# Optimization experiments

Measured on AMD Instinct MI355X. Metric: run time of the kernel, lower is better.

Reference implementation:

```python
import jax, jax.numpy as jnp
import numpy as np

NUM_NET = 5
N = 10000        # nodes per net
E = 160000       # edges per net
B = 512          # molecule graphs per batch
FXD = 62         # node feature dim
FXT = 954        # cell feature dim
D = 128          # output_dim
H1 = 10          # heads in first GATConv


def setup_inputs() -> dict:
    key = jax.random.key(0)
    ks = iter(jax.random.split(key, 64))
    f32 = jnp.float32
    p = lambda shape, scale=0.05: jax.random.normal(next(ks), shape, dtype=f32) * scale
    inp = {}
    inp['x1'] = jax.random.normal(next(ks), (NUM_NET, N, FXD), dtype=f32)
    inp['ei1'] = jax.random.randint(next(ks), (NUM_NET, 2, E), 0, N, dtype=jnp.int32)
    b = ((jnp.arange(N) * B) // N).astype(jnp.int32)  # sorted, no empty graphs
    inp['batch1'] = jnp.broadcast_to(b, (NUM_NET, N))
    inp['x2'] = jax.random.normal(next(ks), (NUM_NET, N, FXD), dtype=f32)
    inp['ei2'] = jax.random.randint(next(ks), (NUM_NET, 2, E), 0, N, dtype=jnp.int32)
    inp['batch2'] = jnp.broadcast_to(b, (NUM_NET, N))
    inp['cell'] = jax.random.normal(next(ks), (B, FXT), dtype=f32)
    # per-net GAT params (stacked over NUM_NET)
    inp['W1'] = p((NUM_NET, H1 * D, FXD))
    inp['a1s'] = p((NUM_NET, H1, D)); inp['a1d'] = p((NUM_NET, H1, D))
    inp['b1'] = p((NUM_NET, H1 * D))
    inp['W2'] = p((NUM_NET, D, H1 * D))
    inp['a2s'] = p((NUM_NET, 1, D)); inp['a2d'] = p((NUM_NET, 1, D))
    inp['b2'] = p((NUM_NET, D))
    inp['Wg'] = p((NUM_NET, D, D)); inp['bg'] = p((NUM_NET, D))
    # cell reduction MLP 954->2048->512->256
    inp['Wr1'] = p((2048, FXT)); inp['br1'] = p((2048,))
    inp['Wr2'] = p((512, 2048)); inp['br2'] = p((512,))
    inp['Wr3'] = p((2 * D, 512)); inp['br3'] = p((2 * D,))
    # head MLP 512->2048->512->128->2
    inp['Wf1'] = p((2048, 4 * D)); inp['bf1'] = p((2048,))
    inp['Wf2'] = p((512, 2048)); inp['bf2'] = p((512,))
    inp['Wf3'] = p((128, 512)); inp['bf3'] = p((128,))
    inp['Wo'] = p((2, 128)); inp['bo'] = p((2,))
    return inp


def _gat(x, src, dst, W, a_s, a_d, b):
    # PyG GATConv (eval): linear -> per-head attention logits -> segment softmax over dst -> scatter-sum
    n = x.shape[0]
    H, C = a_s.shape
    h = (x @ W.T).reshape(n, H, C)
    al = (h * a_s).sum(-1)   # [n, H] source term
    ar = (h * a_d).sum(-1)   # [n, H] dest term
    e = jax.nn.leaky_relu(al[src] + ar[dst], negative_slope=0.2)  # [Ee, H]
    m = jax.ops.segment_max(e, dst, num_segments=n)               # self-loops -> no empty segments
    pe = jnp.exp(e - m[dst])
    s = jax.ops.segment_sum(pe, dst, num_segments=n)
    alpha = pe / s[dst]
    out = jax.ops.segment_sum(h[src] * alpha[:, :, None], dst, num_segments=n)
    return out.reshape(n, H * C) + b


def _branch(x, ei, batch, W1, a1s, a1d, b1, W2, a2s, a2d, b2, Wg, bg):
    n = x.shape[0]
    loops = jnp.arange(n, dtype=ei.dtype)  # add_self_loops=True in PyG GATConv
    src = jnp.concatenate([ei[0], loops])
    dst = jnp.concatenate([ei[1], loops])
    h = jax.nn.elu(_gat(x, src, dst, W1, a1s, a1d, b1))
    h = jax.nn.elu(_gat(h, src, dst, W2, a2s, a2d, b2))
    g = jax.ops.segment_max(h, batch, num_segments=B)  # global max pool
    return jax.nn.relu(g @ Wg.T + bg)


def _l2n(v):
    return v / jnp.clip(jnp.linalg.norm(v, axis=1, keepdims=True), 1e-12)


def reference(x1, ei1, batch1, x2, ei2, batch2, cell,
              W1, a1s, a1d, b1, W2, a2s, a2d, b2, Wg, bg,
              Wr1, br1, Wr2, br2, Wr3, br3,
              Wf1, bf1, Wf2, bf2, Wf3, bf3, Wo, bo):
    x11 = jnp.zeros((B, D), dtype=x1.dtype)
    x22 = jnp.zeros((B, D), dtype=x2.dtype)
    for i in range(NUM_NET):
        pr = (W1[i], a1s[i], a1d[i], b1[i], W2[i], a2s[i], a2d[i], b2[i], Wg[i], bg[i])
        x11 = x11 + _branch(x1[i], ei1[i], batch1[i], *pr) / NUM_NET
        x22 = x22 + _branch(x2[i], ei2[i], batch2[i], *pr) / NUM_NET
    c = _l2n(cell)
    c = jax.nn.relu(c @ Wr1.T + br1)
    c = jax.nn.relu(c @ Wr2.T + br2)
    c = jax.nn.relu(c @ Wr3.T + br3)
    xc = _l2n(jnp.concatenate([x11, x22, c], axis=1))
    xc = jax.nn.relu(xc @ Wf1.T + bf1)
    xc = jax.nn.relu(xc @ Wf2.T + bf2)
    xc = jax.nn.relu(xc @ Wf3.T + bf3)
    return xc @ Wo.T + bo
```

## Files before the change

### kernel.cpp

```cpp
#include <hip/hip_runtime.h>
#include <hip/hip_bf16.h>
#include <math.h>

#define NUM_NET 5
#define NN 10000
#define NE 160000
#define BB 512
#define FXD 62
#define FXT 954
#define MP 10112

typedef __bf16 bf16x8 __attribute__((ext_vector_type(8)));
typedef float f32x4 __attribute__((ext_vector_type(4)));
typedef __hip_bfloat16 bf16;

__device__ __forceinline__ float ldf(const void* p, size_t i) {
  return ((const float*)p)[i];
}
__device__ __forceinline__ float lky(float v) { return v > 0.f ? v : 0.2f * v; }
__device__ __forceinline__ float eluf(float v) { return v > 0.f ? v : (__expf(v) - 1.f); }
__device__ __forceinline__ unsigned int packbf(float a, float b) {
  __hip_bfloat162 t;
  t.x = __float2bfloat16(a);
  t.y = __float2bfloat16(b);
  return *(unsigned int*)&t;
}

struct ConvDesc {
  const void* src;
  bf16* dst;
  int M, K, Mp, Kp, mult, add, batch, pad;
};
struct ConvTable { ConvDesc d[11]; };

__global__ void convert_all_kernel(ConvTable tab) {
  ConvDesc c = tab.d[blockIdx.z];
  int b = blockIdx.y;
  if (b >= c.batch) return;
  int wave = threadIdx.x >> 6, lane = threadIdx.x & 63;
  int r = blockIdx.x * 4 + wave;
  if (r >= c.Mp) return;
  const float* srow = (const float*)c.src + ((size_t)b * c.M + r) * c.K;
  bf16* drow = c.dst + (((size_t)(b * c.mult + c.add)) * c.Mp + r) * c.Kp;
  bool rowok = r < c.M;
  for (int k = lane; k < c.Kp; k += 64) {
    float v = (rowok && k < c.K) ? srow[k] : 0.f;
    drow[k] = __float2bfloat16(v);
  }
}

__global__ void hist_kernel(const int* __restrict__ ei1, const int* __restrict__ ei2,
                            int* __restrict__ counts) {
  int z = blockIdx.z;
  int br = z & 1, net = z >> 1;
  const int* base = (br ? ei2 : ei1) + (size_t)net * 2 * NE;
  const int* dst = base + NE;
  int* cnt = counts + (size_t)z * NN;
  int i = blockIdx.x * 256 + threadIdx.x;
  if (i < NE) atomicAdd(&cnt[dst[i]], 1);
}

__global__ void scan_kernel(const int* __restrict__ counts, int* __restrict__ offs) {
  int z = blockIdx.x;
  counts += (size_t)z * NN;
  offs += (size_t)z * (NN + 1);
  __shared__ int sdata[256];
  __shared__ int s_carry;
  int t = threadIdx.x;
  if (t == 0) { s_carry = 0; offs[0] = 0; }
  __syncthreads();
  for (int base = 0; base < NN; base += 1024) {
    int loc = base + t * 4;
    int v[4];
#pragma unroll
    for (int j = 0; j < 4; j++) v[j] = (loc + j < NN) ? counts[loc + j] : 0;
    int sum4 = v[0] + v[1] + v[2] + v[3];
    sdata[t] = sum4;
    __syncthreads();
    for (int o = 1; o < 256; o <<= 1) {
      int x = (t >= o) ? sdata[t - o] : 0;
      __syncthreads();
      sdata[t] += x;
      __syncthreads();
    }
    int running = sdata[t] - sum4 + s_carry;
#pragma unroll
    for (int j = 0; j < 4; j++) {
      running += v[j];
      if (loc + j < NN) offs[loc + j + 1] = running;
    }
    int tot = sdata[255];
    __syncthreads();
    if (t == 0) s_carry += tot;
    __syncthreads();
  }
}

__global__ void scatter_kernel(const int* __restrict__ ei1, const int* __restrict__ ei2,
                               const int* __restrict__ offs, int* __restrict__ fill,
                               int* __restrict__ csrc) {
  int z = blockIdx.z;
  int br = z & 1, net = z >> 1;
  const int* base = (br ? ei2 : ei1) + (size_t)net * 2 * NE;
  const int* src = base;
  const int* dst = base + NE;
  const int* offz = offs + (size_t)z * (NN + 1);
  int* fillz = fill + (size_t)z * NN;
  int* out = csrc + (size_t)z * NE;
  int i = blockIdx.x * 256 + threadIdx.x;
  if (i < NE) {
    int d = dst[i];
    int p = offz[d] + atomicAdd(&fillz[d], 1);
    out[p] = src[i];
  }
}

__global__ __launch_bounds__(256) void walr_kernel(const void* __restrict__ W1,
                                                   const void* __restrict__ a1s,
                                                   const void* __restrict__ a1d,
                                                   bf16* __restrict__ walrb) {
  int net = blockIdx.x / 10, head = blockIdx.x % 10;
  int t = threadIdx.x, w = t >> 6, k = t & 63;
  __shared__ float ps[8][64];
  float accs = 0.f, accd = 0.f;
  for (int c = w; c < 128; c += 4) {
    float wv = (k < FXD)
        ? ldf(W1, (size_t)net * 1280 * FXD + (size_t)(head * 128 + c) * FXD + k) : 0.f;
    float vs = ldf(a1s, (size_t)net * 1280 + head * 128 + c);
    float vd = ldf(a1d, (size_t)net * 1280 + head * 128 + c);
    accs = fmaf(wv, vs, accs);
    accd = fmaf(wv, vd, accd);
  }
  ps[w][k] = accs;
  ps[4 + w][k] = accd;
  __syncthreads();
  if (w == 0) {
    float s = ps[0][k] + ps[1][k] + ps[2][k] + ps[3][k];
    float dd = ps[4][k] + ps[5][k] + ps[6][k] + ps[7][k];
    walrb[(size_t)net * 4096 + head * 64 + k] = __float2bfloat16(s);
    walrb[(size_t)net * 4096 + (16 + head) * 64 + k] = __float2bfloat16(dd);
  }
}

__global__ __launch_bounds__(256) void alpha_kernel(
    const float* __restrict__ alrA, const int* __restrict__ offsA,
    const int* __restrict__ srcsA, unsigned int* __restrict__ alphaG, int planeBase) {
  int z = blockIdx.z;
  int plane = planeBase + z;
  const float* alr = alrA + (size_t)plane * MP * 32;
  const int* offs = offsA + (size_t)plane * (NN + 1);
  const int* srcs = srcsA + (size_t)plane * NE;
  unsigned int* ag = alphaG + (size_t)z * (NE + NN) * 6;
  int wave = threadIdx.x >> 6, lane = threadIdx.x & 63;
  int d = blockIdx.x * 4 + wave;
  if (d >= NN) return;
  int e0 = offs[d], ne = offs[d + 1] - e0;
  int total = ne + 1;
  float arh[10];
#pragma unroll
  for (int h = 0; h < 10; h++) arh[h] = alr[(size_t)d * 32 + 16 + h];
  if (total <= 64) {
    int sc = (lane < ne) ? srcs[e0 + lane] : d;
    bool act = lane < total;
    const float* ap = &alr[(size_t)sc * 32];
    float v[10], m[10];
#pragma unroll
    for (int h = 0; h < 10; h++) {
      v[h] = act ? lky(ap[h] + arh[h]) : -1e30f;
      m[h] = v[h];
    }
#pragma unroll
    for (int o = 32; o > 0; o >>= 1)
#pragma unroll
      for (int h = 0; h < 10; h++) m[h] = fmaxf(m[h], __shfl_xor(m[h], o));
    float p[10], s[10];
#pragma unroll
    for (int h = 0; h < 10; h++) {
      p[h] = act ? __expf(v[h] - m[h]) : 0.f;
      s[h] = p[h];
    }
#pragma unroll
    for (int o = 32; o > 0; o >>= 1)
#pragma unroll
      for (int h = 0; h < 10; h++) s[h] += __shfl_xor(s[h], o);
    if (act) {
      float inv[10];
#pragma unroll
      for (int h = 0; h < 10; h++) inv[h] = 1.f / s[h];
      unsigned int wv[6];
#pragma unroll
      for (int hp = 0; hp < 5; hp++)
        wv[hp] = packbf(p[2 * hp] * inv[2 * hp], p[2 * hp + 1] * inv[2 * hp + 1]);
      wv[5] = (unsigned int)(d & 15);
      size_t row = (lane < ne) ? (size_t)(e0 + lane) : (size_t)(NE + d);
      unsigned int* rp = ag + row * 6;
#pragma unroll
      for (int j = 0; j < 6; j++) rp[j] = wv[j];
    }
  } else {
    float m[10], s[10];
#pragma unroll
    for (int h = 0; h < 10; h++) { m[h] = -1e30f; s[h] = 0.f; }
    for (int idx = lane; idx < total; idx += 64) {
      int sc = (idx < ne) ? srcs[e0 + idx] : d;
      const float* ap = &alr[(size_t)sc * 32];
#pragma unroll
      for (int h = 0; h < 10; h++) {
        float v = lky(ap[h] + arh[h]);
        if (v > m[h]) { s[h] = s[h] * __expf(m[h] - v) + 1.f; m[h] = v; }
        else s[h] += __expf(v - m[h]);
      }
    }
#pragma unroll
    for (int o = 32; o > 0; o >>= 1)
#pragma unroll
      for (int h = 0; h < 10; h++) {
        float mo = __shfl_xor(m[h], o), so = __shfl_xor(s[h], o);
        if (so > 0.f) {
          if (mo > m[h]) { s[h] = s[h] * __expf(m[h] - mo) + so; m[h] = mo; }
          else s[h] += so * __expf(mo - m[h]);
        }
      }
    for (int idx = lane; idx < total; idx += 64) {
      int sc = (idx < ne) ? srcs[e0 + idx] : d;
      const float* ap = &alr[(size_t)sc * 32];
      unsigned int wv[6];
#pragma unroll
      for (int hp = 0; hp < 5; hp++) {
        float v0 = lky(ap[2 * hp] + arh[2 * hp]);
        float v1 = lky(ap[2 * hp + 1] + arh[2 * hp + 1]);
        wv[hp] = packbf(__expf(v0 - m[2 * hp]) / s[2 * hp],
                        __expf(v1 - m[2 * hp + 1]) / s[2 * hp + 1]);
      }
      wv[5] = (unsigned int)(d & 15);
      size_t row = (idx < ne) ? (size_t)(e0 + idx) : (size_t)(NE + d);
      unsigned int* rp = ag + row * 6;
#pragma unroll
      for (int j = 0; j < 6; j++) rp[j] = wv[j];
    }
  }
}

struct Pref {
  uint4 xv;
  unsigned int a0, a1, a2, a3, a4;
  int dl;
  int av;
};

__device__ __forceinline__ void issue_pref(
    Pref& P, int kb, int e, int fblk, int tid, int nreal, int K_len, int e_begin,
    int d0, const int* __restrict__ srcs, const bf16* __restrict__ xp,
    const unsigned int* __restrict__ ag) {
  int ke = kb + e;
  int src;
  if (ke < nreal) {
    src = srcs[e_begin + ke];
  } else {
    int sl = ke - nreal;
    src = d0 + (sl < 16 ? sl : 0);
  }
  P.xv = *(const uint4*)&xp[(size_t)src * 64 + fblk * 8];
  P.av = 0;
  if (tid < 32 && ke < K_len) {
    P.av = 1;
    size_t row = (ke < nreal) ? (size_t)(e_begin + ke) : (size_t)(NE + d0 + (ke - nreal));
    const unsigned int* rp = ag + row * 6;
    P.a0 = rp[0]; P.a1 = rp[1]; P.a2 = rp[2]; P.a3 = rp[3]; P.a4 = rp[4];
    P.dl = (int)rp[5];
  }
}

__global__ __launch_bounds__(256) void xagg_kernel(
    const bf16* __restrict__ xpadA, const unsigned int* __restrict__ alphaG,
    const int* __restrict__ offsA, const int* __restrict__ srcsA,
    bf16* __restrict__ xagg2, int planeBase) {
  int z = blockIdx.z;
  int plane = planeBase + z;
  bf16* xagg = xagg2 + (size_t)z * 10 * MP * 64;
  int d0 = blockIdx.x * 16;
  int tid = threadIdx.x;

  if (d0 >= NN) {
    uint4 zz; zz.x = zz.y = zz.z = zz.w = 0u;
#pragma unroll
    for (int k = 0; k < 5; k++) {
      int i = tid + k * 256;
      int h = i >> 7, rem = i & 127, row = rem >> 3, seg = rem & 7;
      *(uint4*)&xagg[((size_t)h * MP + d0 + row) * 64 + seg * 8] = zz;
    }
    return;
  }

  const bf16* xp = xpadA + (size_t)plane * MP * 64;
  const int* offs = offsA + (size_t)plane * (NN + 1);
  const int* srcs = srcsA + (size_t)plane * NE;
  const unsigned int* ag = alphaG + (size_t)z * (NE + NN) * 6;

  __shared__ __align__(16) short A_s[10 * 16 * 40];
  __shared__ __align__(16) short Xt_s[64 * 40];

  int e_begin = offs[d0];
  int nreal = offs[d0 + 16] - e_begin;
  int K_len = nreal + 16;

  int e = tid & 31, fblk = tid >> 5;
  int lane = tid & 63, wave = tid >> 6;
  int l15 = lane & 15, quad = lane >> 4;
  int hbase = (wave >> 1) * 5;
  int wcol = (wave & 1) * 32;

  Pref Pn;
  issue_pref(Pn, 0, e, fblk, tid, nreal, K_len, e_begin, d0, srcs, xp, ag);

  {
    f32x4 z4 = (f32x4){0.f, 0.f, 0.f, 0.f};
    for (int i = tid; i < 800; i += 256) ((f32x4*)A_s)[i] = z4;
  }
  f32x4 acc[5][2];
#pragma unroll
  for (int i = 0; i < 5; i++)
#pragma unroll
    for (int j = 0; j < 2; j++) acc[i][j] = (f32x4){0.f, 0.f, 0.f, 0.f};
  int prev_dl = -1;
  __syncthreads();

  for (int kb = 0; kb < K_len; kb += 32) {
    Pref Pc = Pn;
    if (tid < 32) {
      if (prev_dl >= 0) {
#pragma unroll
        for (int h = 0; h < 10; h++) A_s[(h * 16 + prev_dl) * 40 + e] = 0;
      }
      prev_dl = -1;
      if (Pc.av) {
        int dlc = Pc.dl;
        A_s[(0 * 16 + dlc) * 40 + e] = (short)(Pc.a0 & 0xffff);
        A_s[(1 * 16 + dlc) * 40 + e] = (short)(Pc.a0 >> 16);
        A_s[(2 * 16 + dlc) * 40 + e] = (short)(Pc.a1 & 0xffff);
        A_s[(3 * 16 + dlc) * 40 + e] = (short)(Pc.a1 >> 16);
        A_s[(4 * 16 + dlc) * 40 + e] = (short)(Pc.a2 & 0xffff);
        A_s[(5 * 16 + dlc) * 40 + e] = (short)(Pc.a2 >> 16);
        A_s[(6 * 16 + dlc) * 40 + e] = (short)(Pc.a3 & 0xffff);
        A_s[(7 * 16 + dlc) * 40 + e] = (short)(Pc.a3 >> 16);
        A_s[(8 * 16 + dlc) * 40 + e] = (short)(Pc.a4 & 0xffff);
        A_s[(9 * 16 + dlc) * 40 + e] = (short)(Pc.a4 >> 16);
        prev_dl = dlc;
      }
    }
    {
      int fb8 = fblk * 8;
#pragma unroll
      for (int j = 0; j < 4; j++) {
        unsigned int w = ((const unsigned int*)&Pc.xv)[j];
        Xt_s[(fb8 + 2 * j) * 40 + e] = (short)(w & 0xffff);
        Xt_s[(fb8 + 2 * j + 1) * 40 + e] = (short)(w >> 16);
      }
    }
    if (kb + 32 < K_len)
      issue_pref(Pn, kb + 32, e, fblk, tid, nreal, K_len, e_begin, d0, srcs, xp, ag);
    __syncthreads();
    bf16x8 b0 = *(const bf16x8*)&Xt_s[(wcol + l15) * 40 + quad * 8];
    bf16x8 b1 = *(const bf16x8*)&Xt_s[(wcol + 16 + l15) * 40 + quad * 8];
#pragma unroll
    for (int hh = 0; hh < 5; hh++) {
      bf16x8 af = *(const bf16x8*)&A_s[((hbase + hh) * 16 + l15) * 40 + quad * 8];
      acc[hh][0] = __builtin_amdgcn_mfma_f32_16x16x32_bf16(af, b0, acc[hh][0], 0, 0, 0);
      acc[hh][1] = __builtin_amdgcn_mfma_f32_16x16x32_bf16(af, b1, acc[hh][1], 0, 0, 0);
    }
    __syncthreads();
  }

#pragma unroll
  for (int hh = 0; hh < 5; hh++) {
    int h = hbase + hh;
#pragma unroll
    for (int ft = 0; ft < 2; ft++) {
#pragma unroll
      for (int r = 0; r < 4; r++) {
        int drow = d0 + quad * 4 + r;
        xagg[((size_t)h * MP + drow) * 64 + wcol + ft * 16 + l15] =
            __float2bfloat16(acc[hh][ft][r]);
      }
    }
  }
}

__global__ __launch_bounds__(256) void fused_l1l2_kernel(
    const bf16* __restrict__ xagg2, const bf16* __restrict__ W1b,
    const void* __restrict__ b1raw, const bf16* __restrict__ W2b,
    const void* __restrict__ a2s, const void* __restrict__ a2d,
    float* __restrict__ al2A, float* __restrict__ ar2A,
    bf16* __restrict__ h2all, int planeBase) {
  int zz = blockIdx.z;
  int plane = planeBase + zz;
  int net = plane >> 1;
  long ow1 = (long)net * 1280 * 64;
  long ob1 = (long)net * 1280;
  long ow2 = (long)net * 128 * 1280;
  long oa2 = (long)net * 128;
  const bf16* xagg = xagg2 + (size_t)zz * 10 * MP * 64;
  float* al2p = al2A + (size_t)plane * NN;
  float* ar2p = ar2A + (size_t)plane * NN;
  bf16* h2 = h2all + (size_t)plane * MP * 128;
  int r0 = blockIdx.y * 64;
  __shared__ __align__(16) char uraw[52224];
  bf16* Ah = (bf16*)uraw;
  bf16* W1s = Ah + 64 * 72;
  bf16* Ps = (bf16*)uraw;
  bf16* W2s = Ps + 64 * 136;
  __shared__ float s_dot[2][2][32][2];
  int tid = threadIdx.x, lane = tid & 63, wave = tid >> 6;
  int l15 = lane & 15, quad = lane >> 4;
  int rowHalf = wave >> 1, colHalf = wave & 1;
  int wr = rowHalf * 32, wc = colHalf * 64;
  f32x4 acc2[2][4];
#pragma unroll
  for (int i = 0; i < 2; i++)
#pragma unroll
    for (int j = 0; j < 4; j++) acc2[i][j] = (f32x4){0.f, 0.f, 0.f, 0.f};

  for (int h = 0; h < 10; h++) {
    __syncthreads();
    for (int i = tid; i < 512; i += 256) {
      int r = i >> 3, seg = i & 7;
      *(uint4*)&Ah[r * 72 + seg * 8] =
          *(const uint4*)&xagg[((size_t)h * MP + r0 + r) * 64 + seg * 8];
    }
    for (int i = tid; i < 1024; i += 256) {
      int r = i >> 3, seg = i & 7;
      *(uint4*)&W1s[r * 72 + seg * 8] =
          *(const uint4*)&W1b[ow1 + (size_t)(h * 128 + r) * 64 + seg * 8];
    }
    __syncthreads();
    f32x4 acc1[4][2];
#pragma unroll
    for (int i = 0; i < 4; i++)
#pragma unroll
      for (int j = 0; j < 2; j++) acc1[i][j] = (f32x4){0.f, 0.f, 0.f, 0.f};
#pragma unroll
    for (int kc = 0; kc < 2; kc++) {
      bf16x8 af[4], bfr[2];
#pragma unroll
      for (int mi = 0; mi < 4; mi++)
        af[mi] = *(const bf16x8*)&Ah[(mi * 16 + l15) * 72 + kc * 32 + quad * 8];
#pragma unroll
      for (int ni = 0; ni < 2; ni++)
        bfr[ni] = *(const bf16x8*)&W1s[(wave * 32 + ni * 16 + l15) * 72 + kc * 32 + quad * 8];
#pragma unroll
      for (int mi = 0; mi < 4; mi++)
#pragma unroll
        for (int ni = 0; ni < 2; ni++)
          acc1[mi][ni] = __builtin_amdgcn_mfma_f32_16x16x32_bf16(af[mi], bfr[ni], acc1[mi][ni], 0, 0, 0);
    }
    __syncthreads();
#pragma unroll
    for (int ni = 0; ni < 2; ni++) {
      int pcol = wave * 32 + ni * 16 + l15;
      float bv = ldf(b1raw, ob1 + h * 128 + pcol);
#pragma unroll
      for (int mi = 0; mi < 4; mi++)
#pragma unroll
        for (int r = 0; r < 4; r++)
          Ps[(mi * 16 + quad * 4 + r) * 136 + pcol] =
              __float2bfloat16(eluf(acc1[mi][ni][r] + bv));
    }
    for (int i = tid; i < 2048; i += 256) {
      int r = i >> 4, seg = i & 15;
      *(uint4*)&W2s[r * 136 + seg * 8] =
          *(const uint4*)&W2b[ow2 + (size_t)r * 1280 + h * 128 + seg * 8];
    }
    __syncthreads();
#pragma unroll
    for (int kc = 0; kc < 4; kc++) {
      bf16x8 pa[2], pb[4];
#pragma unroll
      for (int mi = 0; mi < 2; mi++)
        pa[mi] = *(const bf16x8*)&Ps[(wr + mi * 16 + l15) * 136 + kc * 32 + quad * 8];
#pragma unroll
      for (int ni = 0; ni < 4; ni++)
        pb[ni] = *(const bf16x8*)&W2s[(wc + ni * 16 + l15) * 136 + kc * 32 + quad * 8];
#pragma unroll
      for (int mi = 0; mi < 2; mi++)
#pragma unroll
        for (int ni = 0; ni < 4; ni++)
          acc2[mi][ni] = __builtin_amdgcn_mfma_f32_16x16x32_bf16(pa[mi], pb[ni], acc2[mi][ni], 0, 0, 0);
    }
  }
  float asv[4], adv[4];
#pragma unroll
  for (int ni = 0; ni < 4; ni++) {
    int col = wc + ni * 16 + l15;
    asv[ni] = ldf(a2s, oa2 + col);
    adv[ni] = ldf(a2d, oa2 + col);
  }
#pragma unroll
  for (int mi = 0; mi < 2; mi++) {
#pragma unroll
    for (int r = 0; r < 4; r++) {
      int rl = mi * 16 + quad * 4 + r;
      int row = r0 + wr + rl;
      float psum = 0.f, pdum = 0.f;
#pragma unroll
      for (int ni = 0; ni < 4; ni++) {
        float v = acc2[mi][ni][r];
        h2[(size_t)row * 128 + wc + ni * 16 + l15] = __float2bfloat16(v);
        psum = fmaf(v, asv[ni], psum);
        pdum = fmaf(v, adv[ni], pdum);
      }
#pragma unroll
      for (int o = 1; o < 16; o <<= 1) {
        psum += __shfl_xor(psum, o);
        pdum += __shfl_xor(pdum, o);
      }
      if (l15 == 0) {
        s_dot[rowHalf][colHalf][rl][0] = psum;
        s_dot[rowHalf][colHalf][rl][1] = pdum;
      }
    }
  }
  __syncthreads();
  if (tid < 64) {
    int row = r0 + tid;
    if (row < NN) {
      int rh = tid >> 5, rl = tid & 31;
      al2p[row] = s_dot[rh][0][rl][0] + s_dot[rh][1][rl][0];
      ar2p[row] = s_dot[rh][0][rl][1] + s_dot[rh][1][rl][1];
    }
  }
}

__global__ __launch_bounds__(256) void mfma_gemm64(
    const bf16* __restrict__ A, long Az, const bf16* __restrict__ B, long Bz, int bdiv,
    const void* __restrict__ bias, long biasoff, long biaszs,
    float* __restrict__ Cf, long Cfz, int ldcf, int accum, int ncols, int brcol,
    bf16* __restrict__ Cb, long Cbz, int ldcb,
    int K, int act, float scale) {
  int z = blockIdx.z;
  int zb = bdiv ? (z >> 1) : z;
  A += (size_t)z * Az;
  B += (size_t)zb * Bz;
  if (Cf) Cf += (size_t)z * Cfz + (size_t)(z & 1) * brcol;
  if (Cb) Cb += (size_t)z * Cbz;
  const bf16* Ag = A + (size_t)blockIdx.y * 64 * K;
  const bf16* Bg = B + (size_t)blockIdx.x * 64 * K;
  __shared__ __align__(16) bf16 Asm[64 * 40];
  __shared__ __align__(16) bf16 Bsm[64 * 40];
  int tid = threadIdx.x;
  int lane = tid & 63, wave = tid >> 6;
  int wr = (wave >> 1) * 32, wc = (wave & 1) * 32;
  int l15 = lane & 15, quad = lane >> 4;
  f32x4 acc[2][2];
#pragma unroll
  for (int i = 0; i < 2; i++)
#pragma unroll
    for (int j = 0; j < 2; j++) acc[i][j] = (f32x4){0.f, 0.f, 0.f, 0.f};
  int isB = tid >> 7;
  int srow = (tid & 127) >> 1, shalf = tid & 1;
  const bf16* G = isB ? Bg : Ag;
  bf16* S = isB ? Bsm : Asm;
  for (int k0 = 0; k0 < K; k0 += 32) {
    const uint4* g = (const uint4*)(G + (size_t)srow * K + k0 + shalf * 16);
    uint4 v0 = g[0], v1 = g[1];
    __syncthreads();
    *(uint4*)&S[srow * 40 + shalf * 16] = v0;
    *(uint4*)&S[srow * 40 + shalf * 16 + 8] = v1;
    __syncthreads();
    bf16x8 af[2], bfr[2];
#pragma unroll
    for (int mi = 0; mi < 2; mi++)
      af[mi] = *(const bf16x8*)&Asm[(wr + mi * 16 + l15) * 40 + quad * 8];
#pragma unroll
    for (int ni = 0; ni < 2; ni++)
      bfr[ni] = *(const bf16x8*)&Bsm[(wc + ni * 16 + l15) * 40 + quad * 8];
#pragma unroll
    for (int mi = 0; mi < 2; mi++)
#pragma unroll
      for (int ni = 0; ni < 2; ni++)
        acc[mi][ni] = __builtin_amdgcn_mfma_f32_16x16x32_bf16(af[mi], bfr[ni], acc[mi][ni], 0, 0, 0);
  }
#pragma unroll
  for (int ni = 0; ni < 2; ni++) {
    int col = blockIdx.x * 64 + wc + ni * 16 + l15;
    if (col >= ncols) continue;
    float bv = bias ? ldf(bias, biasoff + (size_t)zb * biaszs + col) : 0.f;
#pragma unroll
    for (int mi = 0; mi < 2; mi++) {
      int rbase = blockIdx.y * 64 + wr + mi * 16 + quad * 4;
      f32x4 c = acc[mi][ni];
#pragma unroll
      for (int r = 0; r < 4; r++) {
        float v = c[r] + bv;
        if (act == 1) v = fmaxf(v, 0.f);
        else if (act == 2) v = eluf(v);
        v *= scale;
        if (Cf) {
          size_t ci = (size_t)(rbase + r) * ldcf + col;
          if (accum == 1) Cf[ci] += v;
          else if (accum == 2) atomicAdd(&Cf[ci], v);
          else Cf[ci] = v;
        }
        if (Cb) Cb[(size_t)(rbase + r) * ldcb + col] = __float2bfloat16(v);
      }
    }
  }
}

__global__ __launch_bounds__(256) void gat_agg1_kernel(
    const bf16* __restrict__ h2all, const float* __restrict__ alA, const float* __restrict__ arA,
    const int* __restrict__ offsA, const int* __restrict__ srcsA,
    const void* __restrict__ b2, bf16* __restrict__ out2all) {
  int z = blockIdx.z;
  int net = z >> 1;
  const bf16* h = h2all + (size_t)z * MP * 128;
  const float* al = alA + (size_t)z * NN;
  const float* ar = arA + (size_t)z * NN;
  const int* offs = offsA + (size_t)z * (NN + 1);
  const int* srcs = srcsA + (size_t)z * NE;
  __shared__ float2 s_pair[4][64];
  int wave = threadIdx.x >> 6, lane = threadIdx.x & 63;
  int d = blockIdx.x * 4 + wave;
  if (d >= NN) return;
  int e0 = offs[d], ne = offs[d + 1] - e0;
  int total = ne + 1;
  float ard = ar[d];
  float m, s, vcache = -1e30f;
  if (total <= 64) {
    int sc = (lane < ne) ? srcs[e0 + lane] : d;
    bool act = lane < total;
    vcache = act ? lky(al[sc] + ard) : -1e30f;
    m = vcache;
    s = act ? 1.f : 0.f;
#pragma unroll
    for (int o = 32; o > 0; o >>= 1) {
      float mo = __shfl_xor(m, o), so = __shfl_xor(s, o);
      if (so > 0.f) {
        if (mo > m) { s = s * __expf(m - mo) + so; m = mo; }
        else s += so * __expf(mo - m);
      }
    }
  } else {
    m = -1e30f; s = 0.f;
    for (int idx = lane; idx < total; idx += 64) {
      int sc = (idx < ne) ? srcs[e0 + idx] : d;
      float v = lky(al[sc] + ard);
      if (v > m) { s = s * __expf(m - v) + 1.f; m = v; }
      else s += __expf(v - m);
    }
#pragma unroll
    for (int o = 32; o > 0; o >>= 1) {
      float mo = __shfl_xor(m, o), so = __shfl_xor(s, o);
      if (so > 0.f) {
        if (mo > m) { s = s * __expf(m - mo) + so; m = mo; }
        else s += so * __expf(mo - m);
      }
    }
  }
  float inv_s = 1.f / s;
  float acc0 = 0.f, acc1v = 0.f;
  for (int c0 = 0; c0 < total; c0 += 64) {
    int idx = c0 + lane;
    int cnt = min(64, total - c0);
    if (idx < total) {
      int sc = (idx < ne) ? srcs[e0 + idx] : d;
      float v = (total <= 64) ? vcache : lky(al[sc] + ard);
      float a = __expf(v - m) * inv_s;
      s_pair[wave][lane] = make_float2(__int_as_float(sc), a);
    }
    int i = 0;
    for (; i + 2 <= cnt; i += 2) {
      float2 pA = s_pair[wave][i];
      float2 pB = s_pair[wave][i + 1];
      __hip_bfloat162 vA =
          ((const __hip_bfloat162*)(h + (size_t)__float_as_int(pA.x) * 128))[lane];
      __hip_bfloat162 vB =
          ((const __hip_bfloat162*)(h + (size_t)__float_as_int(pB.x) * 128))[lane];
      acc0 = fmaf(__bfloat162float(vA.x), pA.y, acc0);
      acc1v = fmaf(__bfloat162float(vA.y), pA.y, acc1v);
      acc0 = fmaf(__bfloat162float(vB.x), pB.y, acc0);
      acc1v = fmaf(__bfloat162float(vB.y), pB.y, acc1v);
    }
    if (i < cnt) {
      float2 pA = s_pair[wave][i];
      __hip_bfloat162 vA =
          ((const __hip_bfloat162*)(h + (size_t)__float_as_int(pA.x) * 128))[lane];
      acc0 = fmaf(__bfloat162float(vA.x), pA.y, acc0);
      acc1v = fmaf(__bfloat162float(vA.y), pA.y, acc1v);
    }
  }
  float b0 = ldf(b2, (size_t)net * 128 + 2 * lane);
  float b1v = ldf(b2, (size_t)net * 128 + 2 * lane + 1);
  __hip_bfloat162 o;
  o.x = __float2bfloat16(eluf(acc0 + b0));
  o.y = __float2bfloat16(eluf(acc1v + b1v));
  ((__hip_bfloat162*)(out2all + ((size_t)z * NN + d) * 128))[lane] = o;
}

__global__ __launch_bounds__(256) void pool_max_kernel(const bf16* __restrict__ out2all,
                                                       bf16* __restrict__ gall) {
  int z = blockIdx.z;
  const bf16* h = out2all + (size_t)z * NN * 128;
  bf16* g = gall + (size_t)z * BB * 128;
  int wave = threadIdx.x >> 6, lane = threadIdx.x & 63;
  int b = blockIdx.x * 4 + wave;
  if (b >= BB) return;
  int n0 = (b * NN + BB - 1) / BB;
  int n1 = ((b + 1) * NN + BB - 1) / BB;
  if (n1 > NN) n1 = NN;
  float mx = -1e30f, my = -1e30f;
  for (int n = n0; n < n1; n++) {
    __hip_bfloat162 v = ((const __hip_bfloat162*)(h + (size_t)n * 128))[lane];
    mx = fmaxf(mx, __bfloat162float(v.x));
    my = fmaxf(my, __bfloat162float(v.y));
  }
  __hip_bfloat162 o;
  o.x = __float2bfloat16(mx);
  o.y = __float2bfloat16(my);
  ((__hip_bfloat162*)(g + (size_t)b * 128))[lane] = o;
}

__global__ __launch_bounds__(256) void l2norm_b_kernel(const float* __restrict__ x,
                                                       bf16* __restrict__ y, int Din, int Kp) {
  int r = blockIdx.x, t = threadIdx.x;
  __shared__ float red[256];
  float s = 0.f;
  for (int i = t; i < Din; i += 256) {
    float v = x[(size_t)r * Din + i];
    s += v * v;
  }
  red[t] = s;
  __syncthreads();
  for (int o = 128; o > 0; o >>= 1) { if (t < o) red[t] += red[t + o]; __syncthreads(); }
  float inv = 1.f / fmaxf(sqrtf(red[0]), 1e-12f);
  for (int i = t; i < Kp; i += 256) {
    float v = (i < Din) ? x[(size_t)r * Din + i] : 0.f;
    y[(size_t)r * Kp + i] = __float2bfloat16(v * inv);
  }
}

__global__ void final_out_kernel(const float* __restrict__ f3, const void* __restrict__ Wo,
                                 const void* __restrict__ bo, float* __restrict__ out) {
  int r = blockIdx.x;
  int lane = threadIdx.x;
  float x0 = f3[(size_t)r * 128 + lane], x1v = f3[(size_t)r * 128 + 64 + lane];
  float s0 = x0 * ldf(Wo, lane) + x1v * ldf(Wo, 64 + lane);
  float s1 = x0 * ldf(Wo, 128 + lane) + x1v * ldf(Wo, 192 + lane);
#pragma unroll
  for (int o = 32; o > 0; o >>= 1) { s0 += __shfl_down(s0, o); s1 += __shfl_down(s1, o); }
  if (lane == 0) {
    out[r * 2] = s0 + ldf(bo, 0);
    out[r * 2 + 1] = s1 + ldf(bo, 1);
  }
}


extern "C" void kernel_launch(void* const* d_in, const int* in_sizes, int n_in,
                              void* d_out, int out_size, void* d_ws, size_t ws_size,
                              hipStream_t stream) {
  const void* x1 = d_in[0];
  const int* ei1 = (const int*)d_in[1];
  const void* x2 = d_in[3];
  const int* ei2 = (const int*)d_in[4];
  const void* cell = d_in[6];
  const void* W1 = d_in[7];
  const void* a1s = d_in[8];
  const void* a1d = d_in[9];
  const void* b1 = d_in[10];
  const void* W2 = d_in[11];
  const void* a2s = d_in[12];
  const void* a2d = d_in[13];
  const void* b2 = d_in[14];
  const void* Wg = d_in[15];
  const void* bg = d_in[16];
  const void* Wr1 = d_in[17]; const void* br1 = d_in[18];
  const void* Wr2 = d_in[19]; const void* br2 = d_in[20];
  const void* Wr3 = d_in[21]; const void* br3 = d_in[22];
  const void* Wf1 = d_in[23]; const void* bf1 = d_in[24];
  const void* Wf2 = d_in[25]; const void* bf2 = d_in[26];
  const void* Wf3 = d_in[27]; const void* bf3 = d_in[28];
  const void* Wo = d_in[29]; const void* bo = d_in[30];

  char* base = (char*)d_ws;
  size_t off = 0;
  auto alloc = [&](size_t bytes) -> void* {
    void* p = base + off;
    off = (off + bytes + 255) & ~(size_t)255;
    return p;
  };
  bf16* d_xpad = (bf16*)alloc((size_t)10 * MP * 64 * 2);
  bf16* d_W1b = (bf16*)alloc((size_t)5 * 1280 * 64 * 2);
  bf16* d_W2b = (bf16*)alloc((size_t)5 * 128 * 1280 * 2);
  bf16* d_Wgb = (bf16*)alloc((size_t)5 * 128 * 128 * 2);
  bf16* d_Wr1b = (bf16*)alloc((size_t)2048 * 960 * 2);
  bf16* d_Wr2b = (bf16*)alloc((size_t)512 * 2048 * 2);
  bf16* d_Wr3b = (bf16*)alloc((size_t)256 * 512 * 2);
  bf16* d_Wf1b = (bf16*)alloc((size_t)2048 * 512 * 2);
  bf16* d_Wf2b = (bf16*)alloc((size_t)512 * 2048 * 2);
  bf16* d_Wf3b = (bf16*)alloc((size_t)128 * 512 * 2);
  int* d_offs = (int*)alloc((size_t)10 * (NN + 1) * 4);
  int* d_srcs = (int*)alloc((size_t)10 * NE * 4);
  int* d_cnt = (int*)alloc((size_t)10 * NN * 4);
  bf16* d_walrb = (bf16*)alloc((size_t)5 * 64 * 64 * 2);
  float* d_alr = (float*)alloc((size_t)10 * MP * 32 * 4);
  float* d_al2 = (float*)alloc((size_t)20 * NN * 4);
  float* d_ar2 = d_al2 + (size_t)10 * NN;
  bf16* d_h2all = (bf16*)alloc((size_t)10 * MP * 128 * 2);
  unsigned int* d_alphaG = (unsigned int*)alloc((size_t)5 * (NE + NN) * 24);
  char* uni = base + off;
  bf16* d_xagg2 = (bf16*)uni;
  bf16* d_out2all = (bf16*)uni;
  bf16* d_gall = (bf16*)(uni + 25600000);
  float* d_xc = (float*)(uni + 26910720);
  bf16* d_xcb = (bf16*)(uni + 27959296);
  bf16* d_cnb = (bf16*)(uni + 28483584);
  bf16* d_m1b = (bf16*)(uni + 29466624);
  bf16* d_m2b = (bf16*)(uni + 31563776);
  float* d_f3 = (float*)(uni + 32088064);

  ConvTable tab;
  tab.d[0] = {x1, d_xpad, NN, FXD, MP, 64, 2, 0, 5, 0};
  tab.d[1] = {x2, d_xpad, NN, FXD, MP, 64, 2, 1, 5, 0};
  tab.d[2] = {W1, d_W1b, 1280, FXD, 1280, 64, 1, 0, 5, 0};
  tab.d[3] = {W2, d_W2b, 128, 1280, 128, 1280, 1, 0, 5, 0};
  tab.d[4] = {Wg, d_Wgb, 128, 128, 128, 128, 1, 0, 5, 0};
  tab.d[5] = {Wr1, d_Wr1b, 2048, FXT, 2048, 960, 1, 0, 1, 0};
  tab.d[6] = {Wr2, d_Wr2b, 512, 2048, 512, 2048, 1, 0, 1, 0};
  tab.d[7] = {Wr3, d_Wr3b, 256, 512, 256, 512, 1, 0, 1, 0};
  tab.d[8] = {Wf1, d_Wf1b, 2048, 512, 2048, 512, 1, 0, 1, 0};
  tab.d[9] = {Wf2, d_Wf2b, 512, 2048, 512, 2048, 1, 0, 1, 0};
  tab.d[10] = {Wf3, d_Wf3b, 128, 512, 128, 512, 1, 0, 1, 0};
  convert_all_kernel<<<dim3((MP + 3) / 4, 5, 11), 256, 0, stream>>>(tab);

  hipMemsetAsync(d_cnt, 0, (size_t)10 * NN * 4, stream);
  hist_kernel<<<dim3((NE + 255) / 256, 1, 10), 256, 0, stream>>>(ei1, ei2, d_cnt);
  scan_kernel<<<10, 256, 0, stream>>>(d_cnt, d_offs);
  hipMemsetAsync(d_cnt, 0, (size_t)10 * NN * 4, stream);
  scatter_kernel<<<dim3((NE + 255) / 256, 1, 10), 256, 0, stream>>>(ei1, ei2, d_offs, d_cnt, d_srcs);

  walr_kernel<<<50, 256, 0, stream>>>(W1, a1s, a1d, d_walrb);
  mfma_gemm64<<<dim3(1, MP / 64, 10), 256, 0, stream>>>(
      d_xpad, (long)MP * 64, d_walrb, 4096, 1, nullptr, 0, 0,
      d_alr, (long)MP * 32, 32, 0, 32, 0, nullptr, 0, 0, 64, 0, 1.f);

  const int G = 5;
  for (int pb = 0; pb < 10; pb += G) {
    alpha_kernel<<<dim3(NN / 4, 1, G), 256, 0, stream>>>(d_alr, d_offs, d_srcs, d_alphaG, pb);
    xagg_kernel<<<dim3(MP / 16, 1, G), 256, 0, stream>>>(d_xpad, d_alphaG, d_offs, d_srcs, d_xagg2, pb);
    fused_l1l2_kernel<<<dim3(1, MP / 64, G), 256, 0, stream>>>(
        d_xagg2, d_W1b, b1, d_W2b, a2s, a2d, d_al2, d_ar2, d_h2all, pb);
  }

  hipMemsetAsync(d_xc, 0, (size_t)BB * 512 * 4, stream);
  gat_agg1_kernel<<<dim3(2500, 1, 10), 256, 0, stream>>>(
      d_h2all, d_al2, d_ar2, d_offs, d_srcs, b2, d_out2all);
  pool_max_kernel<<<dim3(BB / 4, 1, 10), 256, 0, stream>>>(d_out2all, d_gall);
  mfma_gemm64<<<dim3(2, BB / 64, 10), 256, 0, stream>>>(
      d_gall, (long)BB * 128, d_Wgb, 128 * 128, 1,
      bg, 0, 128,
      d_xc, 0, 512, 2, 128, 128, nullptr, 0, 0, 128, 1, 0.2f);

  l2norm_b_kernel<<<BB, 256, 0, stream>>>((const float*)cell, d_cnb, FXT, 960);
  mfma_gemm64<<<dim3(32, 8, 1), 256, 0, stream>>>(
      d_cnb, 0, d_Wr1b, 0, 0, br1, 0, 0, nullptr, 0, 0, 0, 1 << 30, 0, d_m1b, 0, 2048, 960, 1, 1.f);
  mfma_gemm64<<<dim3(8, 8, 1), 256, 0, stream>>>(
      d_m1b, 0, d_Wr2b, 0, 0, br2, 0, 0, nullptr, 0, 0, 0, 1 << 30, 0, d_m2b, 0, 512, 2048, 1, 1.f);
  mfma_gemm64<<<dim3(4, 8, 1), 256, 0, stream>>>(
      d_m2b, 0, d_Wr3b, 0, 0, br3, 0, 0, d_xc + 256, 0, 512, 0, 1 << 30, 0, nullptr, 0, 0, 512, 1, 1.f);

  l2norm_b_kernel<<<BB, 256, 0, stream>>>(d_xc, d_xcb, 512, 512);
  mfma_gemm64<<<dim3(32, 8, 1), 256, 0, stream>>>(
      d_xcb, 0, d_Wf1b, 0, 0, bf1, 0, 0, nullptr, 0, 0, 0, 1 << 30, 0, d_m1b, 0, 2048, 512, 1, 1.f);
  mfma_gemm64<<<dim3(8, 8, 1), 256, 0, stream>>>(
      d_m1b, 0, d_Wf2b, 0, 0, bf2, 0, 0, nullptr, 0, 0, 0, 1 << 30, 0, d_m2b, 0, 512, 2048, 1, 1.f);
  mfma_gemm64<<<dim3(2, 8, 1), 256, 0, stream>>>(
      d_m2b, 0, d_Wf3b, 0, 0, bf3, 0, 0, d_f3, 0, 128, 0, 1 << 30, 0, nullptr, 0, 0, 512, 1, 1.f);
  final_out_kernel<<<BB, 64, 0, stream>>>(d_f3, Wo, bo, (float*)d_out);
}
```

Before: 1.014 ms.

## Prefetch fused GAT tiles through registers and batch all planes when workspace allows

Inside the fused layer1/layer2 kernel, the next head's xagg and W1 tiles and the current head's W2 tile are now loaded into registers ahead of their LDS stores. This hides global-load latency behind the MFMA work. Separately, the host enlarges the alpha buffer and, if workspace space permits, runs all 10 planes in one group instead of two groups of 5. That cuts launch count and raises per-launch parallelism, at the cost of more register pressure and a larger memory footprint.

Measured after the change: 1.283 ms. 1.27x slower.

```diff
diff --git a/kernel.cpp b/kernel.cpp
--- a/kernel.cpp
+++ b/kernel.cpp
@@ -420,17 +420,34 @@
 #pragma unroll
     for (int j = 0; j < 4; j++) acc2[i][j] = (f32x4){0.f, 0.f, 0.f, 0.f};
 
+  uint4 rA[2], rW1[4], rW2[8];
+#pragma unroll
+  for (int j = 0; j < 2; j++) {
+    int i = tid + j * 256;
+    rA[j] = *(const uint4*)&xagg[((size_t)0 * MP + r0 + (i >> 3)) * 64 + (i & 7) * 8];
+  }
+#pragma unroll
+  for (int j = 0; j < 4; j++) {
+    int i = tid + j * 256;
+    rW1[j] = *(const uint4*)&W1b[ow1 + (size_t)(0 * 128 + (i >> 3)) * 64 + (i & 7) * 8];
+  }
+
   for (int h = 0; h < 10; h++) {
     __syncthreads();
-    for (int i = tid; i < 512; i += 256) {
-      int r = i >> 3, seg = i & 7;
-      *(uint4*)&Ah[r * 72 + seg * 8] =
-          *(const uint4*)&xagg[((size_t)h * MP + r0 + r) * 64 + seg * 8];
-    }
-    for (int i = tid; i < 1024; i += 256) {
-      int r = i >> 3, seg = i & 7;
-      *(uint4*)&W1s[r * 72 + seg * 8] =
-          *(const uint4*)&W1b[ow1 + (size_t)(h * 128 + r) * 64 + seg * 8];
+#pragma unroll
+    for (int j = 0; j < 2; j++) {
+      int i = tid + j * 256;
+      *(uint4*)&Ah[(i >> 3) * 72 + (i & 7) * 8] = rA[j];
+    }
+#pragma unroll
+    for (int j = 0; j < 4; j++) {
+      int i = tid + j * 256;
+      *(uint4*)&W1s[(i >> 3) * 72 + (i & 7) * 8] = rW1[j];
+    }
+#pragma unroll
+    for (int j = 0; j < 8; j++) {
+      int i = tid + j * 256;
+      rW2[j] = *(const uint4*)&W2b[ow2 + (size_t)(i >> 4) * 1280 + h * 128 + (i & 15) * 8];
     }
     __syncthreads();
     f32x4 acc1[4][2];
@@ -465,10 +482,22 @@
           Ps[(mi * 16 + quad * 4 + r) * 136 + pcol] =
               __float2bfloat16(eluf(acc1[mi][ni][r] + bv));
     }
-    for (int i = tid; i < 2048; i += 256) {
-      int r = i >> 4, seg = i & 15;
-      *(uint4*)&W2s[r * 136 + seg * 8] =
-          *(const uint4*)&W2b[ow2 + (size_t)r * 1280 + h * 128 + seg * 8];
+#pragma unroll
+    for (int j = 0; j < 8; j++) {
+      int i = tid + j * 256;
+      *(uint4*)&W2s[(i >> 4) * 136 + (i & 15) * 8] = rW2[j];
+    }
+    if (h < 9) {
+#pragma unroll
+      for (int j = 0; j < 2; j++) {
+        int i = tid + j * 256;
+        rA[j] = *(const uint4*)&xagg[((size_t)(h + 1) * MP + r0 + (i >> 3)) * 64 + (i & 7) * 8];
+      }
+#pragma unroll
+      for (int j = 0; j < 4; j++) {
+        int i = tid + j * 256;
+        rW1[j] = *(const uint4*)&W1b[ow1 + (size_t)((h + 1) * 128 + (i >> 3)) * 64 + (i & 7) * 8];
+      }
     }
     __syncthreads();
 #pragma unroll
@@ -805,8 +834,11 @@
   float* d_al2 = (float*)alloc((size_t)20 * NN * 4);
   float* d_ar2 = d_al2 + (size_t)10 * NN;
   bf16* d_h2all = (bf16*)alloc((size_t)10 * MP * 128 * 2);
-  unsigned int* d_alphaG = (unsigned int*)alloc((size_t)5 * (NE + NN) * 24);
+  unsigned int* d_alphaG = (unsigned int*)alloc((size_t)10 * (NE + NN) * 24);
   char* uni = base + off;
+  size_t avail = (ws_size > off) ? (ws_size - off) : 0;
+  size_t need10 = (size_t)10 * 10 * MP * 64 * 2;
+  int G = (avail >= need10 + 65536) ? 10 : 5;
   bf16* d_xagg2 = (bf16*)uni;
   bf16* d_out2all = (bf16*)uni;
   bf16* d_gall = (bf16*)(uni + 25600000);
@@ -842,7 +874,6 @@
       d_xpad, (long)MP * 64, d_walrb, 4096, 1, nullptr, 0, 0,
       d_alr, (long)MP * 32, 32, 0, 32, 0, nullptr, 0, 0, 64, 0, 1.f);
 
-  const int G = 5;
   for (int pb = 0; pb < 10; pb += G) {
     alpha_kernel<<<dim3(NN / 4, 1, G), 256, 0, stream>>>(d_alr, d_offs, d_srcs, d_alphaG, pb);
     xagg_kernel<<<dim3(MP / 16, 1, G), 256, 0, stream>>>(d_xpad, d_alphaG, d_offs, d_srcs, d_xagg2, pb);
```
